# Kernel tuning notes

Measured on AMD Instinct MI355X. Metric: run time of the kernel, lower is better.

Reference implementation:

```python
import jax, jax.numpy as jnp
import numpy as np

N = 50000      # nodes
E = 800000     # edges (avg degree 16)
IN = 128       # input feature dim
HID = 32       # per-head hidden dim
H = 4          # attention heads
C = 40         # num classes
SLOPE = 0.2    # leaky relu negative slope


def setup_inputs() -> dict:
    key = jax.random.key(0)
    ks = jax.random.split(key, 14)
    s = 0.05
    inputs = jax.random.normal(ks[0], (N, IN), jnp.float32)
    target = jax.random.normal(ks[1], (N, IN), jnp.float32)
    lamb = jax.random.uniform(ks[2], (1,), jnp.float32)
    src = jax.random.randint(ks[3], (E,), 0, N, jnp.int32)
    dst = jax.random.randint(ks[4], (E,), 0, N, jnp.int32)
    W0 = jax.random.normal(ks[5], (IN, H * HID), jnp.float32) * s
    al0 = jax.random.normal(ks[6], (H, HID), jnp.float32) * s
    ar0 = jax.random.normal(ks[7], (H, HID), jnp.float32) * s
    W1 = jax.random.normal(ks[8], (H * HID, H * HID), jnp.float32) * s
    al1 = jax.random.normal(ks[9], (H, HID), jnp.float32) * s
    ar1 = jax.random.normal(ks[10], (H, HID), jnp.float32) * s
    Wout = jax.random.normal(ks[11], (H * HID, C), jnp.float32) * s
    bout = jnp.zeros((C,), jnp.float32)
    return dict(inputs=inputs, target=target, lamb=lamb,
                W0=W0, al0=al0, ar0=ar0, W1=W1, al1=al1, ar1=ar1,
                Wout=Wout, bout=bout, src=src, dst=dst)


def gat_conv(h, W, al, ar, src, dst, residual):
    # h: [N, in_dim]; W: [in_dim, H*HID]; al/ar: [H, HID]
    feat = (h @ W).reshape(N, H, HID)                  # [N,H,D]
    el = jnp.einsum('nhd,hd->nh', feat, al)            # [N,H]
    er = jnp.einsum('nhd,hd->nh', feat, ar)            # [N,H]
    e = jax.nn.leaky_relu(el[src] + er[dst], SLOPE)    # [E,H]
    # edge softmax over incoming edges of each dst node
    emax = jax.ops.segment_max(e, dst, num_segments=N)  # [N,H]
    ee = jnp.exp(e - emax[dst])                          # [E,H]
    denom = jax.ops.segment_sum(ee, dst, num_segments=N)
    a = ee / denom[dst]                                  # [E,H]
    msg = feat[src] * a[:, :, None]                      # [E,H,D]
    out = jax.ops.segment_sum(msg, dst, num_segments=N)  # [N,H,D]
    if residual:
        out = out + h.reshape(N, H, HID)  # identity residual (in == H*HID)
    return jax.nn.elu(out)


def reference(inputs, target, lamb, W0, al0, ar0, W1, al1, ar1, Wout, bout, src, dst):
    def path(x):
        h = gat_conv(x, W0, al0, ar0, src, dst, residual=False).reshape(N, H * HID)
        h = gat_conv(h, W1, al1, ar1, src, dst, residual=True).reshape(N, H * HID)
        return h

    h = path(inputs)
    h2 = path(target)
    lam = lamb[0]
    h = lam * h + (1.0 - lam) * h2   # mixup_hidden=True
    logits = h @ Wout + bout
    return (h, logits)
```

## Files before the change

kernel.cpp:

```cpp
#include <hip/hip_runtime.h>
#include <hip/hip_bf16.h>
#include <cstddef>

#define GN 50000
#define GE 800000
#define GH 4
#define GD 32
#define SLOPE 0.2f
#define LOG2E 1.4426950408889634f

typedef unsigned short ushort_t;
typedef unsigned int uint_t;
using short8 = __attribute__((ext_vector_type(8))) short;
using float4v = __attribute__((ext_vector_type(4))) float;

__device__ __forceinline__ ushort_t f2bf(float f) {
    union { float f; uint_t u; } v; v.f = f;
    uint_t r = v.u + 0x7fff + ((v.u >> 16) & 1);
    return (ushort_t)(r >> 16);
}
__device__ __forceinline__ float bflo(uint_t u) { return __uint_as_float(u << 16); }
__device__ __forceinline__ float bfhi(uint_t u) { return __uint_as_float(u & 0xffff0000u); }
__device__ __forceinline__ float bfu(ushort_t u) { return __uint_as_float((uint_t)u << 16); }

__device__ __forceinline__ uint_t cvt_pk_bf16(float lo, float hi) {
    uint_t r;
    asm("v_cvt_pk_bf16_f32 %0, %1, %2" : "=v"(r) : "v"(lo), "v"(hi));
    return r;
}

#if __has_builtin(__builtin_amdgcn_exp2f)
#define EXP2F(x) __builtin_amdgcn_exp2f(x)
#else
#define EXP2F(x) exp2f(x)
#endif

#define SWZ_B(v, imm) __uint_as_float((uint_t)__builtin_amdgcn_ds_swizzle((int)__float_as_uint(v), (imm)))

__device__ __forceinline__ int slotmap(int a) {
    return (a < GN) ? (a << 1) : (((a - GN) << 1) | 1);
}

__global__ void k_hist(const int* __restrict__ dst, int* __restrict__ deg, int E) {
    int i = blockIdx.x * 256 + threadIdx.x;
    if (i < E) atomicAdd(&deg[dst[i]], 1);
}

__global__ void k_scan1(const int* __restrict__ deg, int* __restrict__ row_ptr,
                        int* __restrict__ partials, int n) {
    __shared__ int s[256];
    int t = threadIdx.x;
    int i = blockIdx.x * 256 + t;
    int v = (i < n) ? deg[i] : 0;
    s[t] = v;
    __syncthreads();
    for (int off = 1; off < 256; off <<= 1) {
        int add = (t >= off) ? s[t - off] : 0;
        __syncthreads();
        s[t] += add;
        __syncthreads();
    }
    if (i < n) row_ptr[i] = s[t] - v;
    if (t == 255) partials[blockIdx.x] = s[255];
}

__global__ void k_scan2(int* __restrict__ partials, int nb) {
    __shared__ int s[256];
    int t = threadIdx.x;
    int v = (t < nb) ? partials[t] : 0;
    s[t] = v;
    __syncthreads();
    for (int off = 1; off < 256; off <<= 1) {
        int add = (t >= off) ? s[t - off] : 0;
        __syncthreads();
        s[t] += add;
        __syncthreads();
    }
    if (t < nb) partials[t] = s[t] - v;
}

__global__ void k_scan3(int* __restrict__ row_ptr, int* __restrict__ wpos,
                        const int* __restrict__ partials, int n, int E) {
    int i = blockIdx.x * 256 + threadIdx.x;
    if (i < n) {
        int rp = row_ptr[i] + partials[i >> 8];
        row_ptr[i] = rp;
        wpos[i] = rp;
        if (i == 0) row_ptr[n] = E;
    }
}

__global__ void k_fill(const int* __restrict__ src, const int* __restrict__ dst,
                       int* __restrict__ wpos, int* __restrict__ csr_src, int E) {
    int i = blockIdx.x * 256 + threadIdx.x;
    if (i < E) {
        int p = atomicAdd(&wpos[dst[i]], 1);
        csr_src[p] = src[i];
    }
}

__global__ void k_cvt_w(const float* __restrict__ W0, const float* __restrict__ W1,
                        ushort_t* __restrict__ wbt) {
    int t = blockIdx.x * 256 + threadIdx.x;
    int m = t >> 14;
    int o = t & 16383;
    int n = o >> 7, k = o & 127;
    const float* W = m ? W1 : W0;
    wbt[t] = f2bf(W[k * 128 + n]);
}

__global__ void k_cvt_wout(const float* __restrict__ Wout, ushort_t* __restrict__ wb) {
    int t = blockIdx.x * 256 + threadIdx.x;
    if (t >= 48 * 128) return;
    int n = t >> 7, k = t & 127;
    float w = (n < 40) ? Wout[k * 40 + n] : 0.f;
    ushort_t h = f2bf(w);
    float r = w - bfu(h);
    wb[t] = h;
    wb[48 * 128 + t] = f2bf(r);
}

__device__ __forceinline__ void lr_epilogue(const float4v acc[2][8],
                                            const float* __restrict__ al,
                                            const float* __restrict__ ar,
                                            float* __restrict__ el,
                                            float* __restrict__ er,
                                            int r0, int quad, int col, int M) {
#pragma unroll
    for (int rt = 0; rt < 2; rt++) {
#pragma unroll
        for (int h = 0; h < 4; h++) {
            float alv0 = al[h * 32 + col], alv1 = al[h * 32 + 16 + col];
            float arv0 = ar[h * 32 + col], arv1 = ar[h * 32 + 16 + col];
            float pl[4], pr[4];
#pragma unroll
            for (int r = 0; r < 4; r++) {
                pl[r] = acc[rt][2 * h][r] * alv0 + acc[rt][2 * h + 1][r] * alv1;
                pr[r] = acc[rt][2 * h][r] * arv0 + acc[rt][2 * h + 1][r] * arv1;
            }
#pragma unroll
            for (int m = 1; m < 16; m <<= 1) {
#pragma unroll
                for (int r = 0; r < 4; r++) {
                    pl[r] += __shfl_xor(pl[r], m, 64);
                    pr[r] += __shfl_xor(pr[r], m, 64);
                }
            }
            if (col == h) {
#pragma unroll
                for (int r = 0; r < 4; r++) {
                    int row = r0 + rt * 16 + quad * 4 + r;
                    if (row < M) el[slotmap(row) * 4 + h] = pl[r] * LOG2E;
                }
            }
            if (col == 8 + h) {
#pragma unroll
                for (int r = 0; r < 4; r++) {
                    int row = r0 + rt * 16 + quad * 4 + r;
                    if (row < M) er[slotmap(row) * 4 + h] = pr[r] * LOG2E;
                }
            }
        }
    }
}

__device__ __forceinline__ void store_c_bf16(ushort_t* __restrict__ Cb,
                                             const float4v acc[2][8],
                                             int r0, int quad, int col, int M) {
#pragma unroll
    for (int rt = 0; rt < 2; rt++)
#pragma unroll
        for (int nt = 0; nt < 8; nt++) {
            int rb = r0 + rt * 16 + quad * 4;
            int c = nt * 16 + col;
            uint_t p01 = cvt_pk_bf16(acc[rt][nt][0], acc[rt][nt][1]);
            uint_t p23 = cvt_pk_bf16(acc[rt][nt][2], acc[rt][nt][3]);
            if (rb + 0 < M) Cb[(size_t)slotmap(rb + 0) * 128 + c] = (ushort_t)p01;
            if (rb + 1 < M) Cb[(size_t)slotmap(rb + 1) * 128 + c] = (ushort_t)(p01 >> 16);
            if (rb + 2 < M) Cb[(size_t)slotmap(rb + 2) * 128 + c] = (ushort_t)p23;
            if (rb + 3 < M) Cb[(size_t)slotmap(rb + 3) * 128 + c] = (ushort_t)(p23 >> 16);
        }
}

__global__ __launch_bounds__(256) void gemm_mfma32(const float* __restrict__ A0,
                                                   const float* __restrict__ A1,
                                                   const ushort_t* __restrict__ WbT,
                                                   const float* __restrict__ al,
                                                   const float* __restrict__ ar,
                                                   ushort_t* __restrict__ Cb,
                                                   float* __restrict__ el,
                                                   float* __restrict__ er, int M) {
    __shared__ ushort_t Bs[128][136];
    int tid = threadIdx.x;
    for (int i = tid; i < 128 * 16; i += 256) {
        int n = i >> 4;
        int kc = (i & 15) << 3;
        *(short8*)&Bs[n][kc] = *(const short8*)&WbT[n * 128 + kc];
    }
    __syncthreads();
    int wid = tid >> 6, lane = tid & 63;
    int r0 = blockIdx.x * 128 + wid * 32;
    int col = lane & 15, quad = lane >> 4;
    float4v acc[2][8];
#pragma unroll
    for (int rt = 0; rt < 2; rt++)
#pragma unroll
        for (int t = 0; t < 8; t++) acc[rt][t] = (float4v){0.f, 0.f, 0.f, 0.f};
    int ar_[2] = {r0 + col, r0 + 16 + col};
    const float* Ap[2];
#pragma unroll
    for (int rt = 0; rt < 2; rt++) {
        int a = ar_[rt];
        Ap[rt] = (a < M) ? ((a < GN) ? (A0 + (size_t)a * 128)
                                     : (A1 + (size_t)(a - GN) * 128)) : nullptr;
    }
#pragma unroll
    for (int ks = 0; ks < 4; ks++) {
        short8 af[2];
#pragma unroll
        for (int rt = 0; rt < 2; rt++) {
            af[rt] = (short8){};
            if (Ap[rt]) {
                float4 v0 = *(const float4*)&Ap[rt][ks * 32 + quad * 8];
                float4 v1 = *(const float4*)&Ap[rt][ks * 32 + quad * 8 + 4];
                union { short8 s; uint_t u[4]; } cv;
                cv.u[0] = cvt_pk_bf16(v0.x, v0.y);
                cv.u[1] = cvt_pk_bf16(v0.z, v0.w);
                cv.u[2] = cvt_pk_bf16(v1.x, v1.y);
                cv.u[3] = cvt_pk_bf16(v1.z, v1.w);
                af[rt] = cv.s;
            }
        }
#pragma unroll
        for (int nt = 0; nt < 8; nt++) {
            short8 bf = *(const short8*)&Bs[nt * 16 + col][ks * 32 + quad * 8];
            acc[0][nt] = __builtin_amdgcn_mfma_f32_16x16x32_bf16(af[0], bf, acc[0][nt], 0, 0, 0);
            acc[1][nt] = __builtin_amdgcn_mfma_f32_16x16x32_bf16(af[1], bf, acc[1][nt], 0, 0, 0);
        }
    }
    store_c_bf16(Cb, acc, r0, quad, col, M);
    lr_epilogue(acc, al, ar, el, er, r0, quad, col, M);
}

__global__ __launch_bounds__(256) void gemm_mfma(const ushort_t* __restrict__ A,
                                                 const ushort_t* __restrict__ WbT,
                                                 const float* __restrict__ al,
                                                 const float* __restrict__ ar,
                                                 ushort_t* __restrict__ Cb,
                                                 float* __restrict__ el,
                                                 float* __restrict__ er, int M) {
    __shared__ ushort_t Bs[128][136];
    int tid = threadIdx.x;
    for (int i = tid; i < 128 * 16; i += 256) {
        int n = i >> 4;
        int kc = (i & 15) << 3;
        *(short8*)&Bs[n][kc] = *(const short8*)&WbT[n * 128 + kc];
    }
    __syncthreads();
    int wid = tid >> 6, lane = tid & 63;
    int r0 = blockIdx.x * 128 + wid * 32;
    int col = lane & 15, quad = lane >> 4;
    float4v acc[2][8];
#pragma unroll
    for (int rt = 0; rt < 2; rt++)
#pragma unroll
        for (int t = 0; t < 8; t++) acc[rt][t] = (float4v){0.f, 0.f, 0.f, 0.f};
    int ar_[2] = {r0 + col, r0 + 16 + col};
    const ushort_t* Ap[2];
#pragma unroll
    for (int rt = 0; rt < 2; rt++) {
        int a = ar_[rt];
        Ap[rt] = (a < M) ? (A + (size_t)slotmap(a) * 128) : nullptr;
    }
#pragma unroll
    for (int ks = 0; ks < 4; ks++) {
        short8 af[2];
#pragma unroll
        for (int rt = 0; rt < 2; rt++) {
            af[rt] = (short8){};
            if (Ap[rt]) af[rt] = *(const short8*)&Ap[rt][ks * 32 + quad * 8];
        }
#pragma unroll
        for (int nt = 0; nt < 8; nt++) {
            short8 bf = *(const short8*)&Bs[nt * 16 + col][ks * 32 + quad * 8];
            acc[0][nt] = __builtin_amdgcn_mfma_f32_16x16x32_bf16(af[0], bf, acc[0][nt], 0, 0, 0);
            acc[1][nt] = __builtin_amdgcn_mfma_f32_16x16x32_bf16(af[1], bf, acc[1][nt], 0, 0, 0);
        }
    }
    store_c_bf16(Cb, acc, r0, quad, col, M);
    lr_epilogue(acc, al, ar, el, er, r0, quad, col, M);
}

__device__ __forceinline__ void agg_core(
    const ushort_t* __restrict__ featb, const float* __restrict__ el, float ern,
    const int* __restrict__ csr_src, int base, int deg, uint_t ebase, uint_t fofs,
    int lane, float& v0, float& v1, float& v2, float& v3) {
    if (deg <= 0) { v0 = v1 = v2 = v3 = 0.f; return; }
    float a0 = 0.f, a1 = 0.f, a2 = 0.f, a3 = 0.f, ss = 0.f;
    int lk = lane & 7;
    int nblk = (deg + 7) >> 3;
    int jb = base;
    int r1 = deg - 1;
    int s0 = csr_src[jb];
    int s1 = csr_src[jb + min(1, r1)];
    int s2 = csr_src[jb + min(2, r1)];
    int s3 = csr_src[jb + min(3, r1)];
    int s4 = csr_src[jb + min(4, r1)];
    int s5 = csr_src[jb + min(5, r1)];
    int s6 = csr_src[jb + min(6, r1)];
    int s7 = csr_src[jb + min(7, r1)];
    int sown = csr_src[jb + min(lk, r1)];
    float eown = el[ebase + (uint_t)sown * 8u];
    int b = 0;
    for (;;) {
        int rem = deg - (b << 3);
        const ushort_t* p0 = featb + (uint_t)s0 * 256u;
        const ushort_t* p1 = featb + (uint_t)s1 * 256u;
        const ushort_t* p2 = featb + (uint_t)s2 * 256u;
        const ushort_t* p3 = featb + (uint_t)s3 * 256u;
        const ushort_t* p4 = featb + (uint_t)s4 * 256u;
        const ushort_t* p5 = featb + (uint_t)s5 * 256u;
        const ushort_t* p6 = featb + (uint_t)s6 * 256u;
        const ushort_t* p7 = featb + (uint_t)s7 * 256u;
        uint2 f0 = *(const uint2*)&p0[fofs];
        uint2 f1 = *(const uint2*)&p1[fofs];
        uint2 f2 = *(const uint2*)&p2[fofs];
        uint2 f3 = *(const uint2*)&p3[fofs];
        uint2 f4 = *(const uint2*)&p4[fofs];
        uint2 f5 = *(const uint2*)&p5[fofs];
        uint2 f6 = *(const uint2*)&p6[fofs];
        uint2 f7 = *(const uint2*)&p7[fofs];
        bool more = (b + 1) < nblk;
        int t0 = 0, t1 = 0, t2 = 0, t3 = 0, t4 = 0, t5 = 0, t6 = 0, t7 = 0, town = 0;
        float eon = 0.f;
        if (more) {
            int nj = jb + 8;
            int r2 = rem - 9;
            t0 = csr_src[nj];
            t1 = csr_src[nj + min(1, r2)];
            t2 = csr_src[nj + min(2, r2)];
            t3 = csr_src[nj + min(3, r2)];
            t4 = csr_src[nj + min(4, r2)];
            t5 = csr_src[nj + min(5, r2)];
            t6 = csr_src[nj + min(6, r2)];
            t7 = csr_src[nj + min(7, r2)];
            town = csr_src[nj + min(lk, r2)];
            eon = el[ebase + (uint_t)town * 8u];
        }
        float e = (lk < rem) ? (eown + ern) : -1e38f;
        e = fmaxf(e, SLOPE * e);
        float wown = EXP2F(e);
        float w0 = SWZ_B(wown, 0x018);
        float w1 = SWZ_B(wown, 0x038);
        float w2 = SWZ_B(wown, 0x058);
        float w3 = SWZ_B(wown, 0x078);
        float w4 = SWZ_B(wown, 0x098);
        float w5 = SWZ_B(wown, 0x0B8);
        float w6 = SWZ_B(wown, 0x0D8);
        float w7 = SWZ_B(wown, 0x0F8);
        ss += ((w0 + w1) + (w2 + w3)) + ((w4 + w5) + (w6 + w7));
        a0 += w0 * bflo(f0.x) + w1 * bflo(f1.x) + w2 * bflo(f2.x) + w3 * bflo(f3.x) +
              w4 * bflo(f4.x) + w5 * bflo(f5.x) + w6 * bflo(f6.x) + w7 * bflo(f7.x);
        a1 += w0 * bfhi(f0.x) + w1 * bfhi(f1.x) + w2 * bfhi(f2.x) + w3 * bfhi(f3.x) +
              w4 * bfhi(f4.x) + w5 * bfhi(f5.x) + w6 * bfhi(f6.x) + w7 * bfhi(f7.x);
        a2 += w0 * bflo(f0.y) + w1 * bflo(f1.y) + w2 * bflo(f2.y) + w3 * bflo(f3.y) +
              w4 * bflo(f4.y) + w5 * bflo(f5.y) + w6 * bflo(f6.y) + w7 * bflo(f7.y);
        a3 += w0 * bfhi(f0.y) + w1 * bfhi(f1.y) + w2 * bfhi(f2.y) + w3 * bfhi(f3.y) +
              w4 * bfhi(f4.y) + w5 * bfhi(f5.y) + w6 * bfhi(f6.y) + w7 * bfhi(f7.y);
        if (!more) break;
        b++; jb += 8;
        s0 = t0; s1 = t1; s2 = t2; s3 = t3; s4 = t4; s5 = t5; s6 = t6; s7 = t7;
        sown = town; eown = eon;
    }
    float inv = 1.f / ss;
    v0 = a0 * inv; v1 = a1 * inv; v2 = a2 * inv; v3 = a3 * inv;
}

__global__ __launch_bounds__(512) void gat_agg_l1(
    const ushort_t* __restrict__ featb, const float* __restrict__ el,
    const float* __restrict__ er, const int* __restrict__ row_ptr,
    const int* __restrict__ csr_src, ushort_t* __restrict__ abuf) {
    int n = __builtin_amdgcn_readfirstlane(blockIdx.x * 8 + (threadIdx.x >> 6));
    if (n >= GN) return;
    int lane = threadIdx.x & 63;
    int half = lane >> 5;
    int q = lane & 31;
    int head = (lane >> 3) & 3, q4 = q << 2;
    uint_t ebase = (uint_t)(half * 4 + head);
    uint_t fofs = (uint_t)(half * 128 + q4);
    float ern = er[(uint_t)n * 8u + ebase];
    int base = row_ptr[n];
    int deg = row_ptr[n + 1] - base;
    float v0, v1, v2, v3;
    agg_core(featb, el, ern, csr_src, base, deg, ebase, fofs, lane, v0, v1, v2, v3);
    v0 = v0 > 0.f ? v0 : __expf(v0) - 1.f;
    v1 = v1 > 0.f ? v1 : __expf(v1) - 1.f;
    v2 = v2 > 0.f ? v2 : __expf(v2) - 1.f;
    v3 = v3 > 0.f ? v3 : __expf(v3) - 1.f;
    size_t idx = ((size_t)(2 * n + half)) * 128 + q4;
    uint2 o;
    o.x = cvt_pk_bf16(v0, v1);
    o.y = cvt_pk_bf16(v2, v3);
    *(uint2*)&abuf[idx] = o;
}

__global__ __launch_bounds__(512) void gat_agg_l2(
    const ushort_t* __restrict__ featb, const float* __restrict__ el,
    const float* __restrict__ er, const int* __restrict__ row_ptr,
    const int* __restrict__ csr_src, const ushort_t* __restrict__ resid,
    const float* __restrict__ lamb, float* __restrict__ outh) {
    int tid = threadIdx.x;
    int n = __builtin_amdgcn_readfirstlane(blockIdx.x * 8 + (tid >> 6));
    if (n >= GN) return;
    int lane = tid & 63;
    int half = lane >> 5;
    int q = lane & 31;
    int head = (lane >> 3) & 3, q4 = q << 2;
    uint_t ebase = (uint_t)(half * 4 + head);
    uint_t fofs = (uint_t)(half * 128 + q4);
    float ern = er[(uint_t)n * 8u + ebase];
    int base = row_ptr[n];
    int deg = row_ptr[n + 1] - base;
    float v0, v1, v2, v3;
    agg_core(featb, el, ern, csr_src, base, deg, ebase, fofs, lane, v0, v1, v2, v3);
    size_t idx = ((size_t)(2 * n + half)) * 128 + q4;
    ushort4 r = *(const ushort4*)&resid[idx];
    v0 += bfu(r.x); v1 += bfu(r.y); v2 += bfu(r.z); v3 += bfu(r.w);
    v0 = v0 > 0.f ? v0 : __expf(v0) - 1.f;
    v1 = v1 > 0.f ? v1 : __expf(v1) - 1.f;
    v2 = v2 > 0.f ? v2 : __expf(v2) - 1.f;
    v3 = v3 > 0.f ? v3 : __expf(v3) - 1.f;
    float p0 = __shfl_xor(v0, 32, 64);
    float p1 = __shfl_xor(v1, 32, 64);
    float p2 = __shfl_xor(v2, 32, 64);
    float p3 = __shfl_xor(v3, 32, 64);
    float lam = lamb[0];
    if (half == 0) {
        float m0 = lam * v0 + (1.f - lam) * p0;
        float m1 = lam * v1 + (1.f - lam) * p1;
        float m2 = lam * v2 + (1.f - lam) * p2;
        float m3 = lam * v3 + (1.f - lam) * p3;
        *(float4*)&outh[(size_t)n * 128 + q4] = make_float4(m0, m1, m2, m3);
    }
}

__global__ __launch_bounds__(256) void k_logits(const float* __restrict__ Hf,
                                                const ushort_t* __restrict__ Wb,
                                                const float* __restrict__ bout,
                                                float* __restrict__ outlog) {
    __shared__ ushort_t Bh[48][136];
    __shared__ ushort_t Bl[48][136];
    int tid = threadIdx.x;
    for (int i = tid; i < 48 * 16; i += 256) {
        int n = i >> 4;
        int kc = (i & 15) << 3;
        *(short8*)&Bh[n][kc] = *(const short8*)&Wb[n * 128 + kc];
        *(short8*)&Bl[n][kc] = *(const short8*)&Wb[48 * 128 + n * 128 + kc];
    }
    __syncthreads();
    int wid = tid >> 6, lane = tid & 63;
    int r0 = blockIdx.x * 128 + wid * 32;
    int col = lane & 15, quad = lane >> 4;
    float4v acc[2][3];
#pragma unroll
    for (int rt = 0; rt < 2; rt++)
#pragma unroll
        for (int nt = 0; nt < 3; nt++) acc[rt][nt] = (float4v){0.f, 0.f, 0.f, 0.f};
    int ar_[2] = {r0 + col, r0 + 16 + col};
#pragma unroll
    for (int ks = 0; ks < 4; ks++) {
        short8 ah[2], alo[2];
#pragma unroll
        for (int rt = 0; rt < 2; rt++) {
            ah[rt] = (short8){};
            alo[rt] = (short8){};
            if (ar_[rt] < GN) {
                const float* p = Hf + (size_t)ar_[rt] * 128 + ks * 32 + quad * 8;
                float4 x = *(const float4*)p;
                float4 y = *(const float4*)(p + 4);
                union { short8 s; uint_t u[4]; } ch, cl;
                ch.u[0] = cvt_pk_bf16(x.x, x.y);
                ch.u[1] = cvt_pk_bf16(x.z, x.w);
                ch.u[2] = cvt_pk_bf16(y.x, y.y);
                ch.u[3] = cvt_pk_bf16(y.z, y.w);
                cl.u[0] = cvt_pk_bf16(x.x - bflo(ch.u[0]), x.y - bfhi(ch.u[0]));
                cl.u[1] = cvt_pk_bf16(x.z - bflo(ch.u[1]), x.w - bfhi(ch.u[1]));
                cl.u[2] = cvt_pk_bf16(y.x - bflo(ch.u[2]), y.y - bfhi(ch.u[2]));
                cl.u[3] = cvt_pk_bf16(y.z - bflo(ch.u[3]), y.w - bfhi(ch.u[3]));
                ah[rt] = ch.s;
                alo[rt] = cl.s;
            }
        }
#pragma unroll
        for (int nt = 0; nt < 3; nt++) {
            short8 bh = *(const short8*)&Bh[nt * 16 + col][ks * 32 + quad * 8];
            short8 bl = *(const short8*)&Bl[nt * 16 + col][ks * 32 + quad * 8];
#pragma unroll
            for (int rt = 0; rt < 2; rt++) {
                acc[rt][nt] = __builtin_amdgcn_mfma_f32_16x16x32_bf16(ah[rt], bh, acc[rt][nt], 0, 0, 0);
                acc[rt][nt] = __builtin_amdgcn_mfma_f32_16x16x32_bf16(alo[rt], bh, acc[rt][nt], 0, 0, 0);
                acc[rt][nt] = __builtin_amdgcn_mfma_f32_16x16x32_bf16(ah[rt], bl, acc[rt][nt], 0, 0, 0);
            }
        }
    }
#pragma unroll
    for (int nt = 0; nt < 3; nt++) {
        int c = nt * 16 + col;
        if (c < 40) {
            float bv = bout[c];
#pragma unroll
            for (int rt = 0; rt < 2; rt++)
#pragma unroll
                for (int r = 0; r < 4; r++) {
                    int row = r0 + rt * 16 + quad * 4 + r;
                    if (row < GN) outlog[(size_t)row * 40 + c] = acc[rt][nt][r] + bv;
                }
        }
    }
}

extern "C" void kernel_launch(void* const* d_in, const int* in_sizes, int n_in,
                              void* d_out, int out_size, void* d_ws, size_t ws_size,
                              hipStream_t stream) {
    const float* inputs = (const float*)d_in[0];
    const float* target = (const float*)d_in[1];
    const float* lamb   = (const float*)d_in[2];
    const float* W0     = (const float*)d_in[3];
    const float* al0    = (const float*)d_in[4];
    const float* ar0    = (const float*)d_in[5];
    const float* W1     = (const float*)d_in[6];
    const float* al1    = (const float*)d_in[7];
    const float* ar1    = (const float*)d_in[8];
    const float* Wout   = (const float*)d_in[9];
    const float* bout   = (const float*)d_in[10];
    const int*   src    = (const int*)d_in[11];
    const int*   dst    = (const int*)d_in[12];

    float* out = (float*)d_out;
    float* outh = out;
    float* outlog = out + (size_t)GN * 128;

    const int NP = 2 * GN;
    ushort_t* featb = (ushort_t*)d_ws;
    ushort_t* abuf  = featb + (size_t)NP * 128;
    float* el = (float*)(abuf + (size_t)NP * 128);
    float* er = el + (size_t)NP * GH;
    ushort_t* wbt = (ushort_t*)(er + (size_t)NP * GH);
    int* row_ptr  = (int*)(wbt + 2 * 128 * 128);
    int* wpos     = row_ptr + (GN + 1);
    int* csr_src  = wpos + GN;
    int* partials = csr_src + GE + 16;
    ushort_t* woutb = (ushort_t*)(partials + 256);

    const int nb = (GN + 255) / 256;
    const int eb = (GE + 255) / 256;
    const int gblocks = (NP + 127) / 128;
    const int aggblocks = (GN + 7) / 8;
    const int lblocks = (GN + 127) / 128;

    hipMemsetAsync(wpos, 0, GN * sizeof(int), stream);
    k_hist<<<eb, 256, 0, stream>>>(dst, wpos, GE);
    k_scan1<<<nb, 256, 0, stream>>>(wpos, row_ptr, partials, GN);
    k_scan2<<<1, 256, 0, stream>>>(partials, nb);
    k_scan3<<<nb, 256, 0, stream>>>(row_ptr, wpos, partials, GN, GE);
    k_fill<<<eb, 256, 0, stream>>>(src, dst, wpos, csr_src, GE);

    k_cvt_w<<<128, 256, 0, stream>>>(W0, W1, wbt);
    k_cvt_wout<<<24, 256, 0, stream>>>(Wout, woutb);

    gemm_mfma32<<<gblocks, 256, 0, stream>>>(inputs, target, wbt, al0, ar0,
                                             featb, el, er, NP);
    gat_agg_l1<<<aggblocks, 512, 0, stream>>>(featb, el, er, row_ptr, csr_src, abuf);

    gemm_mfma<<<gblocks, 256, 0, stream>>>(abuf, wbt + 128 * 128, al1, ar1,
                                           featb, el, er, NP);
    gat_agg_l2<<<aggblocks, 512, 0, stream>>>(featb, el, er, row_ptr, csr_src,
                                              abuf, lamb, outh);

    k_logits<<<lblocks, 256, 0, stream>>>(outh, woutb, bout, outlog);
}
```

Baseline: 406.8 us.

## Recompute source attention logits from gathered features instead of storing el

The GEMM epilogue no longer computes or stores the per-node el logits. Each edge's el is now rebuilt inside the aggregation from the bf16 feature row it already gathers, using a dot product with al and an 8-lane shuffle reduction, which removes a random gather per edge. The aggregation loop is also widened from 8 to 16 edges per block, and the two weight-conversion kernels are merged into one launch. In exchange there are more ALU and shuffle ops per edge and more registers from the 16-wide unroll, and el now comes from bf16-rounded features.

New measurement: 396.5 us. -2.5%, faster.

```diff
diff --git a/kernel.cpp b/kernel.cpp
--- a/kernel.cpp
+++ b/kernel.cpp
@@ -34,8 +34,6 @@
 #else
 #define EXP2F(x) exp2f(x)
 #endif
-
-#define SWZ_B(v, imm) __uint_as_float((uint_t)__builtin_amdgcn_ds_swizzle((int)__float_as_uint(v), (imm)))
 
 __device__ __forceinline__ int slotmap(int a) {
     return (a < GN) ? (a << 1) : (((a - GN) << 1) | 1);
@@ -99,59 +97,45 @@
     }
 }
 
-__global__ void k_cvt_w(const float* __restrict__ W0, const float* __restrict__ W1,
-                        ushort_t* __restrict__ wbt) {
+__global__ void k_cvt_all(const float* __restrict__ W0, const float* __restrict__ W1,
+                          const float* __restrict__ Wout,
+                          ushort_t* __restrict__ wbt, ushort_t* __restrict__ woutb) {
     int t = blockIdx.x * 256 + threadIdx.x;
-    int m = t >> 14;
-    int o = t & 16383;
-    int n = o >> 7, k = o & 127;
-    const float* W = m ? W1 : W0;
-    wbt[t] = f2bf(W[k * 128 + n]);
-}
-
-__global__ void k_cvt_wout(const float* __restrict__ Wout, ushort_t* __restrict__ wb) {
-    int t = blockIdx.x * 256 + threadIdx.x;
-    if (t >= 48 * 128) return;
-    int n = t >> 7, k = t & 127;
-    float w = (n < 40) ? Wout[k * 40 + n] : 0.f;
-    ushort_t h = f2bf(w);
-    float r = w - bfu(h);
-    wb[t] = h;
-    wb[48 * 128 + t] = f2bf(r);
+    if (t < 32768) {
+        int m = t >> 14;
+        int o = t & 16383;
+        int n = o >> 7, k = o & 127;
+        const float* W = m ? W1 : W0;
+        wbt[t] = f2bf(W[k * 128 + n]);
+    } else {
+        int u = t - 32768;
+        if (u < 48 * 128) {
+            int n = u >> 7, k = u & 127;
+            float w = (n < 40) ? Wout[k * 40 + n] : 0.f;
+            ushort_t h = f2bf(w);
+            woutb[u] = h;
+            woutb[48 * 128 + u] = f2bf(w - bfu(h));
+        }
+    }
 }
 
 __device__ __forceinline__ void lr_epilogue(const float4v acc[2][8],
-                                            const float* __restrict__ al,
                                             const float* __restrict__ ar,
-                                            float* __restrict__ el,
                                             float* __restrict__ er,
                                             int r0, int quad, int col, int M) {
 #pragma unroll
     for (int rt = 0; rt < 2; rt++) {
 #pragma unroll
         for (int h = 0; h < 4; h++) {
-            float alv0 = al[h * 32 + col], alv1 = al[h * 32 + 16 + col];
             float arv0 = ar[h * 32 + col], arv1 = ar[h * 32 + 16 + col];
-            float pl[4], pr[4];
-#pragma unroll
-            for (int r = 0; r < 4; r++) {
-                pl[r] = acc[rt][2 * h][r] * alv0 + acc[rt][2 * h + 1][r] * alv1;
+            float pr[4];
+#pragma unroll
+            for (int r = 0; r < 4; r++)
                 pr[r] = acc[rt][2 * h][r] * arv0 + acc[rt][2 * h + 1][r] * arv1;
-            }
 #pragma unroll
             for (int m = 1; m < 16; m <<= 1) {
 #pragma unroll
-                for (int r = 0; r < 4; r++) {
-                    pl[r] += __shfl_xor(pl[r], m, 64);
-                    pr[r] += __shfl_xor(pr[r], m, 64);
-                }
-            }
-            if (col == h) {
-#pragma unroll
-                for (int r = 0; r < 4; r++) {
-                    int row = r0 + rt * 16 + quad * 4 + r;
-                    if (row < M) el[slotmap(row) * 4 + h] = pl[r] * LOG2E;
-                }
+                for (int r = 0; r < 4; r++) pr[r] += __shfl_xor(pr[r], m, 64);
             }
             if (col == 8 + h) {
 #pragma unroll
@@ -185,10 +169,8 @@
 __global__ __launch_bounds__(256) void gemm_mfma32(const float* __restrict__ A0,
                                                    const float* __restrict__ A1,
                                                    const ushort_t* __restrict__ WbT,
-                                                   const float* __restrict__ al,
                                                    const float* __restrict__ ar,
                                                    ushort_t* __restrict__ Cb,
-                                                   float* __restrict__ el,
                                                    float* __restrict__ er, int M) {
     __shared__ ushort_t Bs[128][136];
     int tid = threadIdx.x;
@@ -239,15 +221,13 @@
         }
     }
     store_c_bf16(Cb, acc, r0, quad, col, M);
-    lr_epilogue(acc, al, ar, el, er, r0, quad, col, M);
+    lr_epilogue(acc, ar, er, r0, quad, col, M);
 }
 
 __global__ __launch_bounds__(256) void gemm_mfma(const ushort_t* __restrict__ A,
                                                  const ushort_t* __restrict__ WbT,
-                                                 const float* __restrict__ al,
                                                  const float* __restrict__ ar,
                                                  ushort_t* __restrict__ Cb,
-                                                 float* __restrict__ el,
                                                  float* __restrict__ er, int M) {
     __shared__ ushort_t Bs[128][136];
     int tid = threadIdx.x;
@@ -288,96 +268,60 @@
         }
     }
     store_c_bf16(Cb, acc, r0, quad, col, M);
-    lr_epilogue(acc, al, ar, el, er, r0, quad, col, M);
+    lr_epilogue(acc, ar, er, r0, quad, col, M);
 }
 
 __device__ __forceinline__ void agg_core(
-    const ushort_t* __restrict__ featb, const float* __restrict__ el, float ern,
-    const int* __restrict__ csr_src, int base, int deg, uint_t ebase, uint_t fofs,
-    int lane, float& v0, float& v1, float& v2, float& v3) {
+    const ushort_t* __restrict__ featb, float4 alv, float ern,
+    const int* __restrict__ csr_src, int base, int deg, uint_t fofs,
+    float& v0, float& v1, float& v2, float& v3) {
     if (deg <= 0) { v0 = v1 = v2 = v3 = 0.f; return; }
     float a0 = 0.f, a1 = 0.f, a2 = 0.f, a3 = 0.f, ss = 0.f;
-    int lk = lane & 7;
-    int nblk = (deg + 7) >> 3;
+    int nblk = (deg + 15) >> 4;
     int jb = base;
     int r1 = deg - 1;
-    int s0 = csr_src[jb];
-    int s1 = csr_src[jb + min(1, r1)];
-    int s2 = csr_src[jb + min(2, r1)];
-    int s3 = csr_src[jb + min(3, r1)];
-    int s4 = csr_src[jb + min(4, r1)];
-    int s5 = csr_src[jb + min(5, r1)];
-    int s6 = csr_src[jb + min(6, r1)];
-    int s7 = csr_src[jb + min(7, r1)];
-    int sown = csr_src[jb + min(lk, r1)];
-    float eown = el[ebase + (uint_t)sown * 8u];
+    int s[16], t[16];
+#pragma unroll
+    for (int k = 0; k < 16; k++) s[k] = csr_src[jb + min(k, r1)];
     int b = 0;
     for (;;) {
-        int rem = deg - (b << 3);
-        const ushort_t* p0 = featb + (uint_t)s0 * 256u;
-        const ushort_t* p1 = featb + (uint_t)s1 * 256u;
-        const ushort_t* p2 = featb + (uint_t)s2 * 256u;
-        const ushort_t* p3 = featb + (uint_t)s3 * 256u;
-        const ushort_t* p4 = featb + (uint_t)s4 * 256u;
-        const ushort_t* p5 = featb + (uint_t)s5 * 256u;
-        const ushort_t* p6 = featb + (uint_t)s6 * 256u;
-        const ushort_t* p7 = featb + (uint_t)s7 * 256u;
-        uint2 f0 = *(const uint2*)&p0[fofs];
-        uint2 f1 = *(const uint2*)&p1[fofs];
-        uint2 f2 = *(const uint2*)&p2[fofs];
-        uint2 f3 = *(const uint2*)&p3[fofs];
-        uint2 f4 = *(const uint2*)&p4[fofs];
-        uint2 f5 = *(const uint2*)&p5[fofs];
-        uint2 f6 = *(const uint2*)&p6[fofs];
-        uint2 f7 = *(const uint2*)&p7[fofs];
+        int rem = deg - (b << 4);
+        uint2 f[16];
+#pragma unroll
+        for (int k = 0; k < 16; k++)
+            f[k] = *(const uint2*)&featb[(uint_t)s[k] * 256u + fofs];
         bool more = (b + 1) < nblk;
-        int t0 = 0, t1 = 0, t2 = 0, t3 = 0, t4 = 0, t5 = 0, t6 = 0, t7 = 0, town = 0;
-        float eon = 0.f;
         if (more) {
-            int nj = jb + 8;
-            int r2 = rem - 9;
-            t0 = csr_src[nj];
-            t1 = csr_src[nj + min(1, r2)];
-            t2 = csr_src[nj + min(2, r2)];
-            t3 = csr_src[nj + min(3, r2)];
-            t4 = csr_src[nj + min(4, r2)];
-            t5 = csr_src[nj + min(5, r2)];
-            t6 = csr_src[nj + min(6, r2)];
-            t7 = csr_src[nj + min(7, r2)];
-            town = csr_src[nj + min(lk, r2)];
-            eon = el[ebase + (uint_t)town * 8u];
-        }
-        float e = (lk < rem) ? (eown + ern) : -1e38f;
-        e = fmaxf(e, SLOPE * e);
-        float wown = EXP2F(e);
-        float w0 = SWZ_B(wown, 0x018);
-        float w1 = SWZ_B(wown, 0x038);
-        float w2 = SWZ_B(wown, 0x058);
-        float w3 = SWZ_B(wown, 0x078);
-        float w4 = SWZ_B(wown, 0x098);
-        float w5 = SWZ_B(wown, 0x0B8);
-        float w6 = SWZ_B(wown, 0x0D8);
-        float w7 = SWZ_B(wown, 0x0F8);
-        ss += ((w0 + w1) + (w2 + w3)) + ((w4 + w5) + (w6 + w7));
-        a0 += w0 * bflo(f0.x) + w1 * bflo(f1.x) + w2 * bflo(f2.x) + w3 * bflo(f3.x) +
-              w4 * bflo(f4.x) + w5 * bflo(f5.x) + w6 * bflo(f6.x) + w7 * bflo(f7.x);
-        a1 += w0 * bfhi(f0.x) + w1 * bfhi(f1.x) + w2 * bfhi(f2.x) + w3 * bfhi(f3.x) +
-              w4 * bfhi(f4.x) + w5 * bfhi(f5.x) + w6 * bfhi(f6.x) + w7 * bfhi(f7.x);
-        a2 += w0 * bflo(f0.y) + w1 * bflo(f1.y) + w2 * bflo(f2.y) + w3 * bflo(f3.y) +
-              w4 * bflo(f4.y) + w5 * bflo(f5.y) + w6 * bflo(f6.y) + w7 * bflo(f7.y);
-        a3 += w0 * bfhi(f0.y) + w1 * bfhi(f1.y) + w2 * bfhi(f2.y) + w3 * bfhi(f3.y) +
-              w4 * bfhi(f4.y) + w5 * bfhi(f5.y) + w6 * bfhi(f6.y) + w7 * bfhi(f7.y);
+            int nj = jb + 16;
+            int r2 = rem - 17;
+#pragma unroll
+            for (int k = 0; k < 16; k++) t[k] = csr_src[nj + min(k, r2)];
+        }
+#pragma unroll
+        for (int k = 0; k < 16; k++) {
+            float x0 = bflo(f[k].x), x1 = bfhi(f[k].x);
+            float x2 = bflo(f[k].y), x3 = bfhi(f[k].y);
+            float d = x0 * alv.x + x1 * alv.y + x2 * alv.z + x3 * alv.w;
+            d += __shfl_xor(d, 1, 64);
+            d += __shfl_xor(d, 2, 64);
+            d += __shfl_xor(d, 4, 64);
+            float e = d + ern;
+            e = fmaxf(e, SLOPE * e);
+            float w = (k < rem) ? EXP2F(e) : 0.f;
+            ss += w;
+            a0 += w * x0; a1 += w * x1; a2 += w * x2; a3 += w * x3;
+        }
         if (!more) break;
-        b++; jb += 8;
-        s0 = t0; s1 = t1; s2 = t2; s3 = t3; s4 = t4; s5 = t5; s6 = t6; s7 = t7;
-        sown = town; eown = eon;
+        b++; jb += 16;
+#pragma unroll
+        for (int k = 0; k < 16; k++) s[k] = t[k];
     }
     float inv = 1.f / ss;
     v0 = a0 * inv; v1 = a1 * inv; v2 = a2 * inv; v3 = a3 * inv;
 }
 
 __global__ __launch_bounds__(512) void gat_agg_l1(
-    const ushort_t* __restrict__ featb, const float* __restrict__ el,
+    const ushort_t* __restrict__ featb, const float* __restrict__ al,
     const float* __restrict__ er, const int* __restrict__ row_ptr,
     const int* __restrict__ csr_src, ushort_t* __restrict__ abuf) {
     int n = __builtin_amdgcn_readfirstlane(blockIdx.x * 8 + (threadIdx.x >> 6));
@@ -385,14 +329,15 @@
     int lane = threadIdx.x & 63;
     int half = lane >> 5;
     int q = lane & 31;
-    int head = (lane >> 3) & 3, q4 = q << 2;
-    uint_t ebase = (uint_t)(half * 4 + head);
+    int head = (lane >> 3) & 3, j8 = lane & 7, q4 = q << 2;
+    float4 alv = *(const float4*)&al[head * 32 + j8 * 4];
+    alv.x *= LOG2E; alv.y *= LOG2E; alv.z *= LOG2E; alv.w *= LOG2E;
     uint_t fofs = (uint_t)(half * 128 + q4);
-    float ern = er[(uint_t)n * 8u + ebase];
+    float ern = er[(uint_t)n * 8u + (uint_t)(half * 4 + head)];
     int base = row_ptr[n];
     int deg = row_ptr[n + 1] - base;
     float v0, v1, v2, v3;
-    agg_core(featb, el, ern, csr_src, base, deg, ebase, fofs, lane, v0, v1, v2, v3);
+    agg_core(featb, alv, ern, csr_src, base, deg, fofs, v0, v1, v2, v3);
     v0 = v0 > 0.f ? v0 : __expf(v0) - 1.f;
     v1 = v1 > 0.f ? v1 : __expf(v1) - 1.f;
     v2 = v2 > 0.f ? v2 : __expf(v2) - 1.f;
@@ -405,7 +350,7 @@
 }
 
 __global__ __launch_bounds__(512) void gat_agg_l2(
-    const ushort_t* __restrict__ featb, const float* __restrict__ el,
+    const ushort_t* __restrict__ featb, const float* __restrict__ al,
     const float* __restrict__ er, const int* __restrict__ row_ptr,
     const int* __restrict__ csr_src, const ushort_t* __restrict__ resid,
     const float* __restrict__ lamb, float* __restrict__ outh) {
@@ -415,14 +360,15 @@
     int lane = tid & 63;
     int half = lane >> 5;
     int q = lane & 31;
-    int head = (lane >> 3) & 3, q4 = q << 2;
-    uint_t ebase = (uint_t)(half * 4 + head);
+    int head = (lane >> 3) & 3, j8 = lane & 7, q4 = q << 2;
+    float4 alv = *(const float4*)&al[head * 32 + j8 * 4];
+    alv.x *= LOG2E; alv.y *= LOG2E; alv.z *= LOG2E; alv.w *= LOG2E;
     uint_t fofs = (uint_t)(half * 128 + q4);
-    float ern = er[(uint_t)n * 8u + ebase];
+    float ern = er[(uint_t)n * 8u + (uint_t)(half * 4 + head)];
     int base = row_ptr[n];
     int deg = row_ptr[n + 1] - base;
     float v0, v1, v2, v3;
-    agg_core(featb, el, ern, csr_src, base, deg, ebase, fofs, lane, v0, v1, v2, v3);
+    agg_core(featb, alv, ern, csr_src, base, deg, fofs, v0, v1, v2, v3);
     size_t idx = ((size_t)(2 * n + half)) * 128 + q4;
     ushort4 r = *(const ushort4*)&resid[idx];
     v0 += bfu(r.x); v1 += bfu(r.y); v2 += bfu(r.z); v3 += bfu(r.w);
@@ -543,8 +489,7 @@
     const int NP = 2 * GN;
     ushort_t* featb = (ushort_t*)d_ws;
     ushort_t* abuf  = featb + (size_t)NP * 128;
-    float* el = (float*)(abuf + (size_t)NP * 128);
-    float* er = el + (size_t)NP * GH;
+    float* er = (float*)(abuf + (size_t)NP * 128);
     ushort_t* wbt = (ushort_t*)(er + (size_t)NP * GH);
     int* row_ptr  = (int*)(wbt + 2 * 128 * 128);
     int* wpos     = row_ptr + (GN + 1);
@@ -565,16 +510,15 @@
     k_scan3<<<nb, 256, 0, stream>>>(row_ptr, wpos, partials, GN, GE);
     k_fill<<<eb, 256, 0, stream>>>(src, dst, wpos, csr_src, GE);
 
-    k_cvt_w<<<128, 256, 0, stream>>>(W0, W1, wbt);
-    k_cvt_wout<<<24, 256, 0, stream>>>(Wout, woutb);
-
-    gemm_mfma32<<<gblocks, 256, 0, stream>>>(inputs, target, wbt, al0, ar0,
-                                             featb, el, er, NP);
-    gat_agg_l1<<<aggblocks, 512, 0, stream>>>(featb, el, er, row_ptr, csr_src, abuf);
-
-    gemm_mfma<<<gblocks, 256, 0, stream>>>(abuf, wbt + 128 * 128, al1, ar1,
-                                           featb, el, er, NP);
-    gat_agg_l2<<<aggblocks, 512, 0, stream>>>(featb, el, er, row_ptr, csr_src,
+    k_cvt_all<<<152, 256, 0, stream>>>(W0, W1, Wout, wbt, woutb);
+
+    gemm_mfma32<<<gblocks, 256, 0, stream>>>(inputs, target, wbt, ar0,
+                                             featb, er, NP);
+    gat_agg_l1<<<aggblocks, 512, 0, stream>>>(featb, al0, er, row_ptr, csr_src, abuf);
+
+    gemm_mfma<<<gblocks, 256, 0, stream>>>(abuf, wbt + 128 * 128, ar1,
+                                           featb, er, NP);
+    gat_agg_l2<<<aggblocks, 512, 0, stream>>>(featb, al1, er, row_ptr, csr_src,
                                               abuf, lamb, outh);
 
     k_logits<<<lblocks, 256, 0, stream>>>(outh, woutb, bout, outlog);
```
